# Optimization experiments

Measured on AMD Instinct MI355X. Metric: run time of the kernel, lower is better.

## Reference

```python
import jax, jax.numpy as jnp
import numpy as np


def setup_inputs() -> dict:
    key = jax.random.key(0)
    k1, k2, k3, k4 = jax.random.split(key, 4)
    B, N, d, E = 4, 768, 16, 12288
    emb_nodes = jax.random.normal(k1, (B, N, d), dtype=jnp.float32)
    edges = jax.random.randint(k2, (B, 2, E), 0, N, dtype=jnp.int64)
    # nn.Linear(2*d, 1): weight [1, 2d], bias [1]
    W = jax.random.normal(k3, (2 * d,), dtype=jnp.float32) * 0.1
    b = jax.random.normal(k4, (1,), dtype=jnp.float32) * 0.1
    return {"emb_nodes": emb_nodes, "edges": edges, "W": W, "b": b}


def reference(emb_nodes, edges, W, b):
    B, N, d = emb_nodes.shape
    # all-pairs (i, j): i = repeat_interleave, j = tile  -> [B, N*N, d]
    inter = jnp.repeat(emb_nodes, N, axis=1)
    rep = jnp.tile(emb_nodes, (1, N, 1))
    # original detaches the pair embeddings before the decoder
    edge_embeddings = jax.lax.stop_gradient(jnp.concatenate([inter, rep], axis=-1))  # [B, N*N, 2d]
    logits = edge_embeddings @ W + b[0]  # [B, N*N]
    # self-loop detection via embedding equality (|e_i - e_j| sum == 0)
    non_empty = jnp.abs(inter - rep).sum(axis=-1) != 0
    logits = jnp.where(non_empty, logits, jnp.float32(-10.0))
    # ground-truth edge indicator: scatter 1 at flat index i*N + j
    flat = edges[:, 0] * N + edges[:, 1]  # [B, E]
    truth = jnp.zeros((B, N * N), dtype=emb_nodes.dtype)
    truth = truth.at[jnp.arange(B)[:, None], flat].set(1.0)
    return (edge_embeddings, logits, truth)
```

## Files before the change

### kernel.cpp

```cpp
#include <hip/hip_runtime.h>

constexpr int B = 4;
constexpr int N = 768;
constexpr int D = 16;
constexpr int E = 12288;
constexpr int NN = N * N;
constexpr int PAIRS = B * NN;
constexpr long long EE_FLOATS = (long long)PAIRS * 2 * D;

__global__ void ee_fill_kernel(const float4* __restrict__ emb4,
                               float4* __restrict__ out4, int total4) {
    int idx = blockIdx.x * blockDim.x + threadIdx.x;
    if (idx >= total4) return;
    int pair = idx >> 3;
    int q = idx & 7;
    int b = pair / NN;
    int rem = pair - b * NN;
    int i = rem / N;
    int j = rem - i * N;
    int node = (q < 4) ? i : j;
    out4[idx] = emb4[((b * N + node) << 2) + (q & 3)];
}

__global__ void logits_kernel(const float4* __restrict__ emb4,
                              const float* __restrict__ W,
                              const float* __restrict__ bias,
                              float* __restrict__ logits,
                              float* __restrict__ truth, int total) {
    int p = blockIdx.x * blockDim.x + threadIdx.x;
    if (p >= total) return;
    int b = p / NN;
    int rem = p - b * NN;
    int i = rem / N;
    int j = rem - i * N;
    const float4* ei = emb4 + ((b * N + i) << 2);
    const float4* ej = emb4 + ((b * N + j) << 2);
    float acc = 0.f;
    float diff = 0.f;
#pragma unroll
    for (int q = 0; q < 4; ++q) {
        float4 a = ei[q];
        float4 c = ej[q];
        const float* w1 = W + q * 4;
        const float* w2 = W + D + q * 4;
        acc += a.x * w1[0] + a.y * w1[1] + a.z * w1[2] + a.w * w1[3];
        acc += c.x * w2[0] + c.y * w2[1] + c.z * w2[2] + c.w * w2[3];
        diff += fabsf(a.x - c.x) + fabsf(a.y - c.y) +
                fabsf(a.z - c.z) + fabsf(a.w - c.w);
    }
    acc += bias[0];
    logits[p] = (diff != 0.f) ? acc : -10.0f;
    truth[p] = 0.0f;
}

__global__ void truth_scatter_kernel(const int* __restrict__ edges,
                                     float* __restrict__ truth) {
    int t = blockIdx.x * blockDim.x + threadIdx.x;
    if (t >= B * E) return;
    int b = t / E;
    int e = t - b * E;
    int src = edges[b * 2 * E + e];
    int dst = edges[b * 2 * E + E + e];
    truth[(long long)b * NN + src * N + dst] = 1.0f;
}

extern "C" void kernel_launch(void* const* d_in, const int* in_sizes, int n_in,
                              void* d_out, int out_size, void* d_ws, size_t ws_size,
                              hipStream_t stream) {
    const float4* emb4 = (const float4*)d_in[0];
    const int* edges = (const int*)d_in[1];
    const float* W = (const float*)d_in[2];
    const float* bias = (const float*)d_in[3];

    float* out = (float*)d_out;
    float* ee = out;
    float* logits = out + EE_FLOATS;
    float* truth = out + EE_FLOATS + (long long)PAIRS;

    {
        int total4 = PAIRS * 8;
        int threads = 256;
        int blocks = (total4 + threads - 1) / threads;
        ee_fill_kernel<<<blocks, threads, 0, stream>>>(emb4, (float4*)ee, total4);
    }
    {
        int threads = 256;
        int blocks = (PAIRS + threads - 1) / threads;
        logits_kernel<<<blocks, threads, 0, stream>>>(emb4, W, bias, logits, truth, PAIRS);
    }
    {
        int threads = 256;
        int blocks = (B * E + threads - 1) / threads;
        truth_scatter_kernel<<<blocks, threads, 0, stream>>>(edges, truth);
    }
}
```

Baseline: 333.6 us.

## Fuse edge-embedding fill and logits into one row-per-block kernel

```diff
diff --git a/kernel.cpp b/kernel.cpp
--- a/kernel.cpp
+++ b/kernel.cpp
@@ -8,60 +8,69 @@
 constexpr int PAIRS = B * NN;
 constexpr long long EE_FLOATS = (long long)PAIRS * 2 * D;
 
-__global__ void ee_fill_kernel(const float4* __restrict__ emb4,
-                               float4* __restrict__ out4, int total4) {
-    int idx = blockIdx.x * blockDim.x + threadIdx.x;
-    if (idx >= total4) return;
-    int pair = idx >> 3;
-    int q = idx & 7;
-    int b = pair / NN;
-    int rem = pair - b * NN;
-    int i = rem / N;
-    int j = rem - i * N;
-    int node = (q < 4) ? i : j;
-    out4[idx] = emb4[((b * N + node) << 2) + (q & 3)];
+__device__ __forceinline__ float dot4(float4 a, float4 b) {
+    return a.x * b.x + a.y * b.y + a.z * b.z + a.w * b.w;
+}
+__device__ __forceinline__ float absdiff4(float4 a, float4 b) {
+    return fabsf(a.x - b.x) + fabsf(a.y - b.y) + fabsf(a.z - b.z) + fabsf(a.w - b.w);
 }
 
-__global__ void logits_kernel(const float4* __restrict__ emb4,
-                              const float* __restrict__ W,
-                              const float* __restrict__ bias,
-                              float* __restrict__ logits,
-                              float* __restrict__ truth, int total) {
-    int p = blockIdx.x * blockDim.x + threadIdx.x;
-    if (p >= total) return;
-    int b = p / NN;
-    int rem = p - b * NN;
-    int i = rem / N;
-    int j = rem - i * N;
-    const float4* ei = emb4 + ((b * N + i) << 2);
-    const float4* ej = emb4 + ((b * N + j) << 2);
-    float acc = 0.f;
-    float diff = 0.f;
+__global__ __launch_bounds__(256) void row_fused_kernel(
+    const float4* __restrict__ emb4, const float* __restrict__ W,
+    const float* __restrict__ bias, float4* __restrict__ ee4,
+    float* __restrict__ logits, float* __restrict__ truth) {
+    const int row = blockIdx.x;
+    const int b = row / N;
+    const int i = row - b * N;
+    const float4* __restrict__ eb = emb4 + (size_t)b * N * 4;
+    const float4* __restrict__ ei = eb + i * 4;
+
+    const int t = threadIdx.x;
+    const int q = t & 7;
+    const int qq = q & 3;
+    const bool isI = (q < 4);
+    const float4 eiq = ei[qq];
+
+    float4* __restrict__ orow = ee4 + (size_t)row * (N * 8);
 #pragma unroll
-    for (int q = 0; q < 4; ++q) {
-        float4 a = ei[q];
-        float4 c = ej[q];
-        const float* w1 = W + q * 4;
-        const float* w2 = W + D + q * 4;
-        acc += a.x * w1[0] + a.y * w1[1] + a.z * w1[2] + a.w * w1[3];
-        acc += c.x * w2[0] + c.y * w2[1] + c.z * w2[2] + c.w * w2[3];
-        diff += fabsf(a.x - c.x) + fabsf(a.y - c.y) +
-                fabsf(a.z - c.z) + fabsf(a.w - c.w);
+    for (int k = 0; k < (N * 8) / 256; ++k) {
+        const int f = t + k * 256;
+        float4 v = eiq;
+        if (!isI) v = eb[(f >> 3) * 4 + qq];
+        orow[f] = v;
     }
-    acc += bias[0];
-    logits[p] = (diff != 0.f) ? acc : -10.0f;
-    truth[p] = 0.0f;
+
+    const float4* __restrict__ W4 = (const float4*)W;
+    const float4 wa0 = W4[0], wa1 = W4[1], wa2 = W4[2], wa3 = W4[3];
+    const float4 wb0 = W4[4], wb1 = W4[5], wb2 = W4[6], wb3 = W4[7];
+    const float4 e0 = ei[0], e1 = ei[1], e2 = ei[2], e3 = ei[3];
+    const float base =
+        dot4(e0, wa0) + dot4(e1, wa1) + dot4(e2, wa2) + dot4(e3, wa3) + bias[0];
+    float* __restrict__ lrow = logits + (size_t)row * N;
+    float* __restrict__ trow = truth + (size_t)row * N;
+#pragma unroll
+    for (int k = 0; k < N / 256; ++k) {
+        const int j = t + k * 256;
+        const float4* __restrict__ ej = eb + j * 4;
+        const float4 c0 = ej[0], c1 = ej[1], c2 = ej[2], c3 = ej[3];
+        const float acc = base + dot4(c0, wb0) + dot4(c1, wb1) +
+                          dot4(c2, wb2) + dot4(c3, wb3);
+        const float diff = absdiff4(e0, c0) + absdiff4(e1, c1) +
+                           absdiff4(e2, c2) + absdiff4(e3, c3);
+        lrow[j] = (diff != 0.f) ? acc : -10.0f;
+        trow[j] = 0.0f;
+    }
 }
 
 __global__ void truth_scatter_kernel(const int* __restrict__ edges,
                                      float* __restrict__ truth) {
-    int t = blockIdx.x * blockDim.x + threadIdx.x;
-    if (t >= B * E) return;
-    int b = t / E;
-    int e = t - b * E;
+    int tid = blockIdx.x * blockDim.x + threadIdx.x;
+    if (tid >= B * E) return;
+    int b = tid / E;
+    int e = tid - b * E;
     int src = edges[b * 2 * E + e];
     int dst = edges[b * 2 * E + E + e];
-    truth[(long long)b * NN + src * N + dst] = 1.0f;
+    truth[(size_t)b * NN + src * N + dst] = 1.0f;
 }
 
 extern "C" void kernel_launch(void* const* d_in, const int* in_sizes, int n_in,
@@ -77,20 +86,7 @@
     float* logits = out + EE_FLOATS;
     float* truth = out + EE_FLOATS + (long long)PAIRS;
 
-    {
-        int total4 = PAIRS * 8;
-        int threads = 256;
-        int blocks = (total4 + threads - 1) / threads;
-        ee_fill_kernel<<<blocks, threads, 0, stream>>>(emb4, (float4*)ee, total4);
-    }
-    {
-        int threads = 256;
-        int blocks = (PAIRS + threads - 1) / threads;
-        logits_kernel<<<blocks, threads, 0, stream>>>(emb4, W, bias, logits, truth, PAIRS);
-    }
-    {
-        int threads = 256;
-        int blocks = (B * E + threads - 1) / threads;
-        truth_scatter_kernel<<<blocks, threads, 0, stream>>>(edges, truth);
-    }
+    row_fused_kernel<<<B * N, 256, 0, stream>>>(emb4, W, bias, (float4*)ee,
+                                                logits, truth);
+    truth_scatter_kernel<<<(B * E + 255) / 256, 256, 0, stream>>>(edges, truth);
 }
```

Result: no change. 335.2 us (+0.5%).
